# Performance work log

Hardware: AMD Instinct MI355X
Metric: run time of the kernel (lower is better)

## Reference

```python
import jax, jax.numpy as jnp
import numpy as np

N = 4096
E = 262144
IN_C = 128
OUT_C = 128
EDGE_D = 16


def setup_inputs() -> dict:
    key = jax.random.key(0)
    k = jax.random.split(key, 8)
    x = jax.random.normal(k[0], (N, IN_C), dtype=jnp.float32)
    edge_index = jax.random.randint(k[1], (2, E), 0, N, dtype=jnp.int64)
    edge_attr = jax.random.normal(k[2], (N, N, EDGE_D), dtype=jnp.float32)
    # nn.Linear params: y = x @ W.T + b; store pre-transposed W for x @ W
    s1 = 1.0 / np.sqrt(IN_C + EDGE_D)
    s2 = 1.0 / np.sqrt(OUT_C)
    W1 = jax.random.uniform(k[3], (IN_C + EDGE_D, OUT_C), jnp.float32, -s1, s1)
    b1 = jax.random.uniform(k[4], (OUT_C,), jnp.float32, -s1, s1)
    W2 = jax.random.uniform(k[5], (OUT_C, OUT_C), jnp.float32, -s2, s2)
    b2 = jax.random.uniform(k[6], (OUT_C,), jnp.float32, -s2, s2)
    return {"x": x, "edge_index": edge_index, "edge_attr": edge_attr,
            "W1": W1, "b1": b1, "W2": W2, "b2": b2}


def reference(x, edge_index, edge_attr, W1, b1, W2, b2):
    row, col = edge_index[0], edge_index[1]
    x_row = x[row]                      # [E, IN_C] gather
    e = edge_attr[row, col]             # [E, EDGE_D] gather from dense NxN table
    h = jnp.concatenate([x_row, e], axis=-1)     # [E, IN_C+EDGE_D]
    h = jax.nn.relu(h @ W1 + b1)                  # [E, OUT_C]
    h = jax.nn.relu(h @ W2 + b2)                  # [E, OUT_C]
    # global_add_pool(out, col): scatter-add edges into node buckets by col
    return jax.ops.segment_sum(h, col, num_segments=x.shape[0])  # [N, OUT_C]
```

## Files before the change

kernel.cpp:

```cpp
#include <hip/hip_runtime.h>
#include <hip/hip_bf16.h>

#define NN 4096
#define IC 128
#define OC 128
#define ED 16
#define EPB 128
#define NT 512
#define NSLOT 8
#define NBLK 256

typedef __bf16 bf16x8 __attribute__((ext_vector_type(8)));
typedef float  f32x4  __attribute__((ext_vector_type(4)));

#define BAR() do { asm volatile("s_waitcnt lgkmcnt(0)" ::: "memory"); \
    __builtin_amdgcn_s_barrier(); \
    __builtin_amdgcn_sched_barrier(0); } while (0)

__device__ __forceinline__ unsigned short bf16u(float f) {
    unsigned int u = __float_as_uint(f);
    u = (u + 0x7FFFu + ((u >> 16) & 1u)) >> 16;
    return (unsigned short)u;
}
__device__ __forceinline__ float bf16tof(unsigned short h) {
    return __uint_as_float(((unsigned int)h) << 16);
}
__device__ __forceinline__ int swzk(int row) { return (row ^ (row >> 3)) & 7; }

__global__ __launch_bounds__(128) void k_xw1(
    const float* __restrict__ x, const float* __restrict__ W1,
    const float* __restrict__ b1, float* __restrict__ xw1b)
{
    __shared__ float xs[8][IC];
    const int t = threadIdx.x;
    const int r0 = blockIdx.x * 8;
    #pragma unroll
    for (int r = 0; r < 8; ++r) xs[r][t] = x[(size_t)(r0 + r) * IC + t];
    __syncthreads();
    float acc[8];
    const float bb = b1[t];
    #pragma unroll
    for (int r = 0; r < 8; ++r) acc[r] = bb;
    #pragma unroll 4
    for (int k = 0; k < IC; ++k) {
        const float w = W1[(size_t)k * OC + t];
        #pragma unroll
        for (int r = 0; r < 8; ++r) acc[r] = fmaf(xs[r][k], w, acc[r]);
    }
    #pragma unroll
    for (int r = 0; r < 8; ++r) xw1b[(size_t)(r0 + r) * OC + t] = acc[r];
}

__global__ void k_hist(const int* __restrict__ eidx, int* __restrict__ hist, int E) {
    const int i = blockIdx.x * blockDim.x + threadIdx.x;
    if (i < E) atomicAdd(&hist[eidx[E + i]], 1);
}

__global__ __launch_bounds__(256) void k_scan(
    const int* __restrict__ hist, int* __restrict__ cursor)
{
    __shared__ int tot[256];
    __shared__ int base[256];
    const int t = threadIdx.x;
    int loc[16];
    int s = 0;
    #pragma unroll
    for (int j = 0; j < 16; ++j) { loc[j] = s; s += hist[t * 16 + j]; }
    tot[t] = s;
    __syncthreads();
    if (t == 0) {
        int a = 0;
        for (int i = 0; i < 256; ++i) { base[i] = a; a += tot[i]; }
    }
    __syncthreads();
    const int b = base[t];
    #pragma unroll
    for (int j = 0; j < 16; ++j) cursor[t * 16 + j] = b + loc[j];
}

__global__ void k_scatter(const int* __restrict__ eidx, int* __restrict__ cursor,
                          int2* __restrict__ csr, int E) {
    const int i = blockIdx.x * blockDim.x + threadIdx.x;
    if (i < E) {
        const int row = eidx[i];
        const int col = eidx[E + i];
        const int pos = atomicAdd(&cursor[col], 1);
        csr[pos] = make_int2(row, col);
    }
}

__global__ __launch_bounds__(NT, 2) void k_edge5(
    const int2* __restrict__ csr, const float* __restrict__ eattr,
    const float* __restrict__ xw1b, const float* __restrict__ W1,
    const float* __restrict__ W2, const float* __restrict__ b2,
    float* __restrict__ out, int E)
{
    extern __shared__ char smem[];
    char*   const W2hi = smem;
    char*   const W2lo = smem + 32768;
    char*   const h1hi = smem + 65536;
    char*   const h1lo = smem + 98304;
    float4* const eaL  = (float4*)(smem + 131072);
    float4* const w1L  = (float4*)(smem + 139264);
    float*  const lacc = (float*)(smem + 147456);
    int*    const srowL = (int*)(smem + 151552);
    int*    const scolL = srowL + 256;

    const int t   = threadIdx.x;
    const int l   = t & 63;
    const int wid = t >> 6;
    const int cg  = t & 15, eg = t >> 4;
    const int c0  = cg << 3, e0 = eg << 2;
    const int sz  = (eg >> 1) & 3;
    const int em  = t >> 2, q = t & 3;
    const int esz = (em >> 3) & 3;

    w1L[t] = ((const float4*)(W1 + (size_t)IC * OC))[t];
    {
        const int n = t >> 2, kh = (t & 3) * 32;
        const int key = swzk(n) << 4;
        for (int j0 = 0; j0 < 32; j0 += 8) {
            union { unsigned short us[8]; uint4 qv; } Hh, Hl;
            #pragma unroll
            for (int j = 0; j < 8; ++j) {
                const float w = W2[(size_t)(kh + j0 + j) * OC + n];
                const unsigned short h = bf16u(w);
                Hh.us[j] = h;
                Hl.us[j] = bf16u(w - bf16tof(h));
            }
            const int a = n * 256 + (((kh + j0) * 2) ^ key);
            *(uint4*)(W2hi + a) = Hh.qv;
            *(uint4*)(W2lo + a) = Hl.qv;
        }
    }
    float b2r[8];
    #pragma unroll
    for (int nr = 0; nr < 8; ++nr) b2r[nr] = b2[nr * 16 + (l & 15)];

    const int nper = (E / EPB) / NBLK;
    const int ibb  = blockIdx.x * nper;

    if (t < EPB) {
        const int2 rc = csr[(size_t)ibb * EPB + t];
        srowL[t] = rc.x;
        scolL[t] = rc.y;
    }
    __syncthreads();

    float4 pA;
    {
        const int r = srowL[em], c = scolL[em];
        pA = ((const float4*)(eattr + ((size_t)r * NN + c) * ED))[q];
    }

    int cur = 0;
    for (int ii = 0; ii < nper; ++ii) {
        const int ib  = ibb + ii;
        const int nxt = cur ^ 1;

        BAR();

        int2 idxn;
        {
            const int ibn = (ii + 1 < nper) ? (ib + 1) : ib;
            idxn = (t < EPB) ? csr[(size_t)ibn * EPB + t] : make_int2(0, 0);
        }
        lacc[t] = 0.f; lacc[t + NT] = 0.f;
        if (t < EPB) { srowL[nxt * 128 + t] = idxn.x; scolL[nxt * 128 + t] = idxn.y; }
        eaL[(em * 4 + q) ^ esz] = pA;
        float4 xa[4], xb[4];
        #pragma unroll
        for (int ri = 0; ri < 4; ++ri) {
            const int row = srowL[cur * 128 + e0 + ri];
            const float4* p = (const float4*)(xw1b + (size_t)row * OC + c0);
            xa[ri] = p[0]; xb[ri] = p[1];
        }
        BAR();

        float4 ha[4], hb[4];
        #pragma unroll
        for (int ri = 0; ri < 4; ++ri) { ha[ri] = xa[ri]; hb[ri] = xb[ri]; }
        #pragma unroll
        for (int dc = 0; dc < 4; ++dc) {
            float4 ev[4];
            #pragma unroll
            for (int ri = 0; ri < 4; ++ri)
                ev[ri] = eaL[((e0 + ri) * 4 + dc) ^ sz];
            #pragma unroll
            for (int dd = 0; dd < 4; ++dd) {
                const int d = dc * 4 + dd;
                const float4 wA = w1L[d * 32 + cg * 2];
                const float4 wB = w1L[d * 32 + cg * 2 + 1];
                #pragma unroll
                for (int ri = 0; ri < 4; ++ri) {
                    const float evd = (dd == 0) ? ev[ri].x : (dd == 1) ? ev[ri].y
                                     : (dd == 2) ? ev[ri].z : ev[ri].w;
                    ha[ri].x = fmaf(evd, wA.x, ha[ri].x);
                    ha[ri].y = fmaf(evd, wA.y, ha[ri].y);
                    ha[ri].z = fmaf(evd, wA.z, ha[ri].z);
                    ha[ri].w = fmaf(evd, wA.w, ha[ri].w);
                    hb[ri].x = fmaf(evd, wB.x, hb[ri].x);
                    hb[ri].y = fmaf(evd, wB.y, hb[ri].y);
                    hb[ri].z = fmaf(evd, wB.z, hb[ri].z);
                    hb[ri].w = fmaf(evd, wB.w, hb[ri].w);
                }
            }
        }
        #pragma unroll
        for (int ri = 0; ri < 4; ++ri) {
            const int row = e0 + ri;
            float v[8] = { ha[ri].x, ha[ri].y, ha[ri].z, ha[ri].w,
                           hb[ri].x, hb[ri].y, hb[ri].z, hb[ri].w };
            union { unsigned short us[8]; uint4 qv; } Hh, Hl;
            #pragma unroll
            for (int j = 0; j < 8; ++j) {
                const float f = fmaxf(v[j], 0.f);
                const unsigned short h = bf16u(f);
                Hh.us[j] = h;
                Hl.us[j] = bf16u(f - bf16tof(h));
            }
            const int boff = (cg * 16) ^ (swzk(row) << 4);
            *(uint4*)(h1hi + row * 256 + boff) = Hh.qv;
            *(uint4*)(h1lo + row * 256 + boff) = Hl.qv;
        }
        {
            const int r = srowL[nxt * 128 + em], c = scolL[nxt * 128 + em];
            pA = ((const float4*)(eattr + ((size_t)r * NN + c) * ED))[q];
        }
        BAR();

        f32x4 acc[8];
        #pragma unroll
        for (int nr = 0; nr < 8; ++nr) acc[nr] = (f32x4){0.f, 0.f, 0.f, 0.f};
        const int arow = wid * 16 + (l & 15);
        const int akey = swzk(arow) << 4;
        #pragma unroll
        for (int kc = 0; kc < 4; ++kc) {
            const int kb = kc * 64 + ((l >> 4) << 4);
            const bf16x8 aH = *(const bf16x8*)(h1hi + arow * 256 + (kb ^ akey));
            const bf16x8 aL = *(const bf16x8*)(h1lo + arow * 256 + (kb ^ akey));
            #pragma unroll
            for (int nr = 0; nr < 8; ++nr) {
                const int brow = nr * 16 + (l & 15);
                const int ba = brow * 256 + (kb ^ (swzk(brow) << 4));
                const bf16x8 bH = *(const bf16x8*)(W2hi + ba);
                const bf16x8 bL = *(const bf16x8*)(W2lo + ba);
                acc[nr] = __builtin_amdgcn_mfma_f32_16x16x32_bf16(aH, bH, acc[nr], 0, 0, 0);
                acc[nr] = __builtin_amdgcn_mfma_f32_16x16x32_bf16(aL, bH, acc[nr], 0, 0, 0);
                acc[nr] = __builtin_amdgcn_mfma_f32_16x16x32_bf16(aH, bL, acc[nr], 0, 0, 0);
            }
        }

        const int colbase = scolL[cur * 128];
        {
            const int eb = wid * 16 + ((l >> 4) << 2);
            float s[8];
            int ccur = scolL[cur * 128 + eb];
            #pragma unroll
            for (int nr = 0; nr < 8; ++nr)
                s[nr] = fmaxf(acc[nr][0] + b2r[nr], 0.f);
            #pragma unroll
            for (int r = 1; r < 4; ++r) {
                const int c = scolL[cur * 128 + eb + r];
                if (c != ccur) {
                    const int slot = ccur - colbase;
                    if (slot < NSLOT) {
                        #pragma unroll
                        for (int nr = 0; nr < 8; ++nr)
                            if (s[nr] != 0.f)
                                atomicAdd(&lacc[slot * OC + nr * 16 + (l & 15)], s[nr]);
                    } else {
                        #pragma unroll
                        for (int nr = 0; nr < 8; ++nr)
                            if (s[nr] != 0.f)
                                atomicAdd(&out[(size_t)ccur * OC + nr * 16 + (l & 15)], s[nr]);
                    }
                    ccur = c;
                    #pragma unroll
                    for (int nr = 0; nr < 8; ++nr)
                        s[nr] = fmaxf(acc[nr][r] + b2r[nr], 0.f);
                } else {
                    #pragma unroll
                    for (int nr = 0; nr < 8; ++nr)
                        s[nr] += fmaxf(acc[nr][r] + b2r[nr], 0.f);
                }
            }
            {
                const int slot = ccur - colbase;
                if (slot < NSLOT) {
                    #pragma unroll
                    for (int nr = 0; nr < 8; ++nr)
                        if (s[nr] != 0.f)
                            atomicAdd(&lacc[slot * OC + nr * 16 + (l & 15)], s[nr]);
                } else {
                    #pragma unroll
                    for (int nr = 0; nr < 8; ++nr)
                        if (s[nr] != 0.f)
                            atomicAdd(&out[(size_t)ccur * OC + nr * 16 + (l & 15)], s[nr]);
                }
            }
        }
        BAR();

        int span = scolL[cur * 128 + 127] - colbase + 1;
        if (span > NSLOT) span = NSLOT;
        for (int idx = t; idx < span * OC; idx += NT) {
            const float v = lacc[idx];
            if (v != 0.f)
                atomicAdd(&out[(size_t)(colbase + (idx >> 7)) * OC + (idx & 127)], v);
        }
        cur = nxt;
    }
}

#define LDS_BYTES 153600

extern "C" void kernel_launch(void* const* d_in, const int* in_sizes, int n_in,
                              void* d_out, int out_size, void* d_ws, size_t ws_size,
                              hipStream_t stream) {
    const float* x    = (const float*)d_in[0];
    const int*   eidx = (const int*)d_in[1];
    const float* ea   = (const float*)d_in[2];
    const float* W1   = (const float*)d_in[3];
    const float* b1   = (const float*)d_in[4];
    const float* W2   = (const float*)d_in[5];
    const float* b2   = (const float*)d_in[6];
    float* out = (float*)d_out;

    const int E = in_sizes[1] / 2;

    char* ws = (char*)d_ws;
    float* xw1b   = (float*)ws;
    int*   hist   = (int*)(ws + 2097152);
    int*   cursor = (int*)(ws + 2097152 + 16384);
    int2*  csr    = (int2*)(ws + 2097152 + 32768);

    hipMemsetAsync(d_out, 0, (size_t)out_size * sizeof(float), stream);
    hipMemsetAsync(hist, 0, 4096 * sizeof(int), stream);

    k_xw1<<<NN / 8, 128, 0, stream>>>(x, W1, b1, xw1b);
    k_hist<<<(E + 255) / 256, 256, 0, stream>>>(eidx, hist, E);
    k_scan<<<1, 256, 0, stream>>>(hist, cursor);
    k_scatter<<<(E + 255) / 256, 256, 0, stream>>>(eidx, cursor, csr, E);

    hipFuncSetAttribute(reinterpret_cast<const void*>(k_edge5),
                        hipFuncAttributeMaxDynamicSharedMemorySize, LDS_BYTES);
    k_edge5<<<NBLK, NT, LDS_BYTES, stream>>>(csr, ea, xw1b, W1, W2, b2, out, E);
}
```

Measured before the change: 155.5 us.

## Prefetch next tile's xw1b rows and CSR indices; fold memsets into xw1 kernel

Moves the gather of xw1b rows for the next edge tile and the CSR index load two tiles ahead into the previous iteration, so these global loads overlap with the second-layer MFMA work instead of stalling the start of each tile. It also removes two hipMemsetAsync calls by zeroing the output and histogram inside the k_xw1 kernel. The prefetch adds register pressure (xa/xb held across the MFMA stage) at a launch bound of 2 blocks per CU.

```diff
diff --git a/kernel.cpp b/kernel.cpp
--- a/kernel.cpp
+++ b/kernel.cpp
@@ -29,13 +29,25 @@
 
 __global__ __launch_bounds__(128) void k_xw1(
     const float* __restrict__ x, const float* __restrict__ W1,
-    const float* __restrict__ b1, float* __restrict__ xw1b)
+    const float* __restrict__ b1, float* __restrict__ xw1b,
+    float* __restrict__ out, int* __restrict__ hist)
 {
     __shared__ float xs[8][IC];
     const int t = threadIdx.x;
     const int r0 = blockIdx.x * 8;
     #pragma unroll
     for (int r = 0; r < 8; ++r) xs[r][t] = x[(size_t)(r0 + r) * IC + t];
+
+    const float4 z = make_float4(0.f, 0.f, 0.f, 0.f);
+    float4* o4 = (float4*)out;
+    o4[blockIdx.x * 256 + t]       = z;
+    o4[blockIdx.x * 256 + 128 + t] = z;
+    if (blockIdx.x == 0) {
+        int4* h4 = (int4*)hist;
+        #pragma unroll
+        for (int j = 0; j < 8; ++j) h4[j * 128 + t] = make_int4(0, 0, 0, 0);
+    }
+
     __syncthreads();
     float acc[8];
     const float bb = b1[t];
@@ -89,7 +101,7 @@
     }
 }
 
-__global__ __launch_bounds__(NT, 2) void k_edge5(
+__global__ __launch_bounds__(NT, 2) void k_edge6(
     const int2* __restrict__ csr, const float* __restrict__ eattr,
     const float* __restrict__ xw1b, const float* __restrict__ W1,
     const float* __restrict__ W2, const float* __restrict__ b2,
@@ -152,29 +164,28 @@
         const int r = srowL[em], c = scolL[em];
         pA = ((const float4*)(eattr + ((size_t)r * NN + c) * ED))[q];
     }
+    float4 xa[4], xb[4];
+    #pragma unroll
+    for (int ri = 0; ri < 4; ++ri) {
+        const int row = srowL[e0 + ri];
+        const float4* p = (const float4*)(xw1b + (size_t)row * OC + c0);
+        xa[ri] = p[0]; xb[ri] = p[1];
+    }
+    int2 pidx;
+    {
+        const int ibn = (nper > 1) ? 1 : 0;
+        pidx = (t < EPB) ? csr[(size_t)(ibb + ibn) * EPB + t] : make_int2(0, 0);
+    }
 
     int cur = 0;
     for (int ii = 0; ii < nper; ++ii) {
-        const int ib  = ibb + ii;
         const int nxt = cur ^ 1;
 
         BAR();
 
-        int2 idxn;
-        {
-            const int ibn = (ii + 1 < nper) ? (ib + 1) : ib;
-            idxn = (t < EPB) ? csr[(size_t)ibn * EPB + t] : make_int2(0, 0);
-        }
         lacc[t] = 0.f; lacc[t + NT] = 0.f;
-        if (t < EPB) { srowL[nxt * 128 + t] = idxn.x; scolL[nxt * 128 + t] = idxn.y; }
+        if (t < EPB) { srowL[nxt * 128 + t] = pidx.x; scolL[nxt * 128 + t] = pidx.y; }
         eaL[(em * 4 + q) ^ esz] = pA;
-        float4 xa[4], xb[4];
-        #pragma unroll
-        for (int ri = 0; ri < 4; ++ri) {
-            const int row = srowL[cur * 128 + e0 + ri];
-            const float4* p = (const float4*)(xw1b + (size_t)row * OC + c0);
-            xa[ri] = p[0]; xb[ri] = p[1];
-        }
         BAR();
 
         float4 ha[4], hb[4];
@@ -223,9 +234,20 @@
             *(uint4*)(h1hi + row * 256 + boff) = Hh.qv;
             *(uint4*)(h1lo + row * 256 + boff) = Hl.qv;
         }
+
         {
             const int r = srowL[nxt * 128 + em], c = scolL[nxt * 128 + em];
             pA = ((const float4*)(eattr + ((size_t)r * NN + c) * ED))[q];
+        }
+        #pragma unroll
+        for (int ri = 0; ri < 4; ++ri) {
+            const int row = srowL[nxt * 128 + e0 + ri];
+            const float4* p = (const float4*)(xw1b + (size_t)row * OC + c0);
+            xa[ri] = p[0]; xb[ri] = p[1];
+        }
+        {
+            const int iin = (ii + 2 < nper) ? (ii + 2) : (nper - 1);
+            pidx = (t < EPB) ? csr[(size_t)(ibb + iin) * EPB + t] : make_int2(0, 0);
         }
         BAR();
 
@@ -335,15 +357,12 @@
     int*   cursor = (int*)(ws + 2097152 + 16384);
     int2*  csr    = (int2*)(ws + 2097152 + 32768);
 
-    hipMemsetAsync(d_out, 0, (size_t)out_size * sizeof(float), stream);
-    hipMemsetAsync(hist, 0, 4096 * sizeof(int), stream);
-
-    k_xw1<<<NN / 8, 128, 0, stream>>>(x, W1, b1, xw1b);
+    k_xw1<<<NN / 8, 128, 0, stream>>>(x, W1, b1, xw1b, out, hist);
     k_hist<<<(E + 255) / 256, 256, 0, stream>>>(eidx, hist, E);
     k_scan<<<1, 256, 0, stream>>>(hist, cursor);
     k_scatter<<<(E + 255) / 256, 256, 0, stream>>>(eidx, cursor, csr, E);
 
-    hipFuncSetAttribute(reinterpret_cast<const void*>(k_edge5),
+    hipFuncSetAttribute(reinterpret_cast<const void*>(k_edge6),
                         hipFuncAttributeMaxDynamicSharedMemorySize, LDS_BYTES);
-    k_edge5<<<NBLK, NT, LDS_BYTES, stream>>>(csr, ea, xw1b, W1, W2, b2, out, E);
-}
+    k_edge6<<<NBLK, NT, LDS_BYTES, stream>>>(csr, ea, xw1b, W1, W2, b2, out, E);
+}
```

After: 151.6 us. 2.5% less time.
